# Kernel tuning notes

Measured on AMD Instinct MI355X. Metric: run time of the kernel, lower is better.

The kernel has to match this reference:

```python
import jax, jax.numpy as jnp
import numpy as np

B, T, D, S = 32, 4096, 64, 128


def setup_inputs() -> dict:
    key = jax.random.key(0)
    ks = jax.random.split(key, 6)
    return {
        "observations": jax.random.normal(ks[0], (B, T, D), jnp.float32),
        "trans_logits": jax.random.normal(ks[1], (S, S), jnp.float32),
        "w1": jax.random.normal(ks[2], (4 * S, D), jnp.float32) / np.sqrt(D).astype(np.float32),
        "b1": jnp.zeros((4 * S,), jnp.float32),
        "w2": jax.random.normal(ks[3], (S, 4 * S), jnp.float32) / np.sqrt(4 * S).astype(np.float32),
        "b2": jnp.zeros((S,), jnp.float32),
        "init_logits": jax.random.normal(ks[4], (S,), jnp.float32),
    }


def _hmm_posteriors(observations, trans_logits, w1, b1, w2, b2):
    # observations: (batch, seq, obs_dim) -> (seq, batch, obs_dim)
    obs = jnp.transpose(observations, (1, 0, 2))
    # Emission MLP is time-independent: precompute all emission logits at once.
    hid = jax.nn.relu(jnp.einsum('tbd,hd->tbh', obs, w1) + b1)
    emit = jnp.einsum('tbh,sh->tbs', hid, w2) + b2  # (T, B, S)

    log_trans_f = jax.nn.log_softmax(trans_logits, axis=-1)      # forward cell
    log_trans_b = jax.nn.log_softmax(trans_logits.T, axis=-1)    # backward cell (transposed logits)

    bsz = observations.shape[0]
    n_states = trans_logits.shape[0]
    h0 = jnp.zeros((bsz, n_states), emit.dtype)

    def make_step(log_trans):
        def step(prev, e):
            nxt = jax.scipy.special.logsumexp(prev[:, :, None] + log_trans[None], axis=1) + e
            return nxt, nxt
        return step

    _, log_alphas = jax.lax.scan(make_step(log_trans_f), h0, emit)
    _, betas_rev = jax.lax.scan(make_step(log_trans_b), h0, emit[::-1])
    log_betas = betas_rev[::-1]

    log_Z = jax.scipy.special.logsumexp(log_alphas[-1], axis=-1)  # (B,)
    log_gammas = log_alphas + log_betas - log_Z[None, :, None]
    posteriors = jax.nn.softmax(log_gammas, axis=-1)              # (T, B, S)
    return jnp.transpose(posteriors, (1, 0, 2))                   # (B, T, S)


def reference(observations, trans_logits, w1, b1, w2, b2, init_logits):
    # init_logits is a declared parameter of HMMModel but is unused in forward.
    return _hmm_posteriors(observations, trans_logits, w1, b1, w2, b2)
```

## Files before the change

### kernel.cpp

```cpp
#include <hip/hip_runtime.h>
#include <hip/hip_bf16.h>
#include <stdint.h>

#define BB 32
#define TT 4096
#define DD 64
#define SS 128
#define HH 512

#define SC_W 8
#define SC_L 32

typedef __attribute__((ext_vector_type(4))) float f32x4;
typedef __attribute__((ext_vector_type(8))) short s16x8;
typedef __attribute__((ext_vector_type(4))) short s16x4;

__device__ __forceinline__ ushort f2bfu(float x) {
    uint32_t b = __float_as_uint(x);
    uint32_t r = (b + 0x7FFFu + ((b >> 16) & 1u)) >> 16;
    return (ushort)r;
}
__device__ __forceinline__ float bfu2f(ushort u) {
    return __uint_as_float(((uint32_t)u) << 16);
}

__global__ __launch_bounds__(128) void prep_trans(const float* __restrict__ tr,
                                                  float* __restrict__ PfT,
                                                  float* __restrict__ PbT) {
    int i = blockIdx.x & 127;
    int back = blockIdx.x >> 7;
    int j = threadIdx.x;
    float v = back ? tr[j * SS + i] : tr[i * SS + j];
    __shared__ float sh[4];
    float mx = v;
#pragma unroll
    for (int off = 32; off; off >>= 1) mx = fmaxf(mx, __shfl_xor(mx, off));
    if ((threadIdx.x & 63) == 0) sh[threadIdx.x >> 6] = mx;
    __syncthreads();
    mx = fmaxf(sh[0], sh[1]);
    float e = __expf(v - mx);
    float ssum = e;
#pragma unroll
    for (int off = 32; off; off >>= 1) ssum += __shfl_xor(ssum, off);
    if ((threadIdx.x & 63) == 0) sh[2 + (threadIdx.x >> 6)] = ssum;
    __syncthreads();
    float out = e / (sh[2] + sh[3]);
    if (back) PbT[j * SS + i] = out;
    else      PfT[j * SS + i] = out;
}

__global__ __launch_bounds__(256) void conv_w(const float* __restrict__ w1,
                                              const float* __restrict__ w2,
                                              ushort* __restrict__ w1f,
                                              ushort* __restrict__ w2f) {
    int i = blockIdx.x * 256 + threadIdx.x;
    if (i < 4096) {
        int f1 = i >> 6, l = i & 63;
        int kt = f1 & 1, htile = f1 >> 1;
        int row = htile * 16 + (l & 15);
        int col = kt * 32 + (l >> 4) * 8;
        const float* src = w1 + row * DD + col;
        ushort* dst = w1f + i * 8;
#pragma unroll
        for (int j = 0; j < 8; ++j) dst[j] = f2bfu(src[j]);
    } else if (i < 4096 + 8192) {
        int i2 = i - 4096;
        int f2 = i2 >> 6, l = i2 & 63;
        int kt = f2 & 15, si = (f2 >> 4) & 1, sg = f2 >> 5;
        int row = sg * 32 + si * 16 + (l & 15);
        int col = kt * 32 + (l >> 4) * 8;
        const float* src = w2 + row * HH + col;
        ushort* dst = w2f + i2 * 8;
#pragma unroll
        for (int j = 0; j < 8; ++j) dst[j] = f2bfu(src[j]);
    }
}

#define MLP_ROWS 64
__global__ __launch_bounds__(512, 4) void mlp_kernel(
    const float* __restrict__ obs, const ushort* __restrict__ w1f,
    const ushort* __restrict__ w2f, const float* __restrict__ b1,
    const float* __restrict__ b2, ushort* __restrict__ emitb) {
    __shared__ __align__(16) ushort Alds[MLP_ROWS][72];
    __shared__ __align__(16) ushort Hlds[MLP_ROWS][524];

    int wg = blockIdx.x;
    int bb = wg >> 6;
    int t0 = (wg & 63) * MLP_ROWS;
    int tid = threadIdx.x;
    int lane = tid & 63, wv = tid >> 6;
    int lhi = lane >> 4, llo = lane & 15;

    {
        int r = tid >> 3, c0 = (tid & 7) * 8;
        const float* src = obs + ((size_t)bb * TT + t0 + r) * DD + c0;
        float4 v0 = *(const float4*)(src);
        float4 v1 = *(const float4*)(src + 4);
        s16x8 pk;
        pk[0] = (short)f2bfu(v0.x); pk[1] = (short)f2bfu(v0.y);
        pk[2] = (short)f2bfu(v0.z); pk[3] = (short)f2bfu(v0.w);
        pk[4] = (short)f2bfu(v1.x); pk[5] = (short)f2bfu(v1.y);
        pk[6] = (short)f2bfu(v1.z); pk[7] = (short)f2bfu(v1.w);
        *(s16x8*)(&Alds[r][c0]) = pk;
    }
    __syncthreads();

    int h0 = wv * 64;
    f32x4 acc1[4][4];
#pragma unroll
    for (int mi = 0; mi < 4; ++mi)
#pragma unroll
        for (int nt = 0; nt < 4; ++nt) acc1[mi][nt] = (f32x4){0.f, 0.f, 0.f, 0.f};
#pragma unroll
    for (int kt = 0; kt < 2; ++kt) {
        s16x8 wf1[4];
#pragma unroll
        for (int mi = 0; mi < 4; ++mi) {
            int htile = wv * 4 + mi;
            wf1[mi] = *(const s16x8*)(w1f + ((htile * 2 + kt) * 64 + lane) * 8);
        }
#pragma unroll
        for (int nt = 0; nt < 4; ++nt) {
            s16x8 of = *(const s16x8*)(&Alds[nt * 16 + llo][kt * 32 + lhi * 8]);
#pragma unroll
            for (int mi = 0; mi < 4; ++mi)
                acc1[mi][nt] = __builtin_amdgcn_mfma_f32_16x16x32_bf16(wf1[mi], of, acc1[mi][nt], 0, 0, 0);
        }
    }
#pragma unroll
    for (int mi = 0; mi < 4; ++mi) {
        float4 b1v = *(const float4*)(b1 + h0 + mi * 16 + lhi * 4);
#pragma unroll
        for (int nt = 0; nt < 4; ++nt) {
            s16x4 pk;
            pk[0] = (short)f2bfu(fmaxf(acc1[mi][nt][0] + b1v.x, 0.f));
            pk[1] = (short)f2bfu(fmaxf(acc1[mi][nt][1] + b1v.y, 0.f));
            pk[2] = (short)f2bfu(fmaxf(acc1[mi][nt][2] + b1v.z, 0.f));
            pk[3] = (short)f2bfu(fmaxf(acc1[mi][nt][3] + b1v.w, 0.f));
            *(s16x4*)(&Hlds[nt * 16 + llo][h0 + mi * 16 + lhi * 4]) = pk;
        }
    }

    int sg = wv >> 1, th = wv & 1;
    int sb = sg * 32;
    s16x8 wfr2[4][2];
#pragma unroll
    for (int kp = 0; kp < 4; ++kp)
#pragma unroll
        for (int si = 0; si < 2; ++si)
            wfr2[kp][si] = *(const s16x8*)(w2f + ((sg * 32 + si * 16 + kp) * 64 + lane) * 8);

    __syncthreads();

    f32x4 acc2[2][2];
#pragma unroll
    for (int si = 0; si < 2; ++si)
#pragma unroll
        for (int nt = 0; nt < 2; ++nt) acc2[si][nt] = (f32x4){0.f, 0.f, 0.f, 0.f};
#pragma unroll
    for (int kt = 0; kt < 16; ++kt) {
        s16x8 hf[2];
#pragma unroll
        for (int nt = 0; nt < 2; ++nt)
            hf[nt] = *(const s16x8*)(&Hlds[th * 32 + nt * 16 + llo][kt * 32 + lhi * 8]);
#pragma unroll
        for (int si = 0; si < 2; ++si)
#pragma unroll
            for (int nt = 0; nt < 2; ++nt)
                acc2[si][nt] = __builtin_amdgcn_mfma_f32_16x16x32_bf16(wfr2[kt & 3][si], hf[nt], acc2[si][nt], 0, 0, 0);
        if (kt < 12) {
#pragma unroll
            for (int si = 0; si < 2; ++si)
                wfr2[kt & 3][si] = *(const s16x8*)(w2f + ((sg * 32 + si * 16 + (kt + 4)) * 64 + lane) * 8);
        }
    }
#pragma unroll
    for (int si = 0; si < 2; ++si) {
        int sbase = sb + si * 16 + lhi * 4;
        float4 b2v = *(const float4*)(b2 + sbase);
#pragma unroll
        for (int nt = 0; nt < 2; ++nt) {
            int tl = th * 32 + nt * 16 + llo;
            ushort* dst = emitb + ((size_t)bb * TT + t0 + tl) * SS + sbase;
            s16x4 pk;
            pk[0] = (short)f2bfu(__expf(acc2[si][nt][0] + b2v.x));
            pk[1] = (short)f2bfu(__expf(acc2[si][nt][1] + b2v.y));
            pk[2] = (short)f2bfu(__expf(acc2[si][nt][2] + b2v.z));
            pk[3] = (short)f2bfu(__expf(acc2[si][nt][3] + b2v.w));
            *(s16x4*)dst = pk;
        }
    }
}

__global__ __launch_bounds__(256, 2) void scan_mfma(
    const ushort* __restrict__ Eb, const float* __restrict__ PfT,
    const float* __restrict__ PbT, ushort* __restrict__ galpha,
    ushort* __restrict__ gbeta) {
    int wg = blockIdx.x;
    int b = wg >> 4;
    int dir = (wg >> 3) & 1;
    int wgc = wg & 7;
    int resetRow = (dir == 0) ? (wgc == 0 ? 0 : -1) : (wgc == 7 ? 15 : -1);
    int tid = threadIdx.x;
    int l = tid & 63, w = tid >> 6;
    int l15 = l & 15, g = l >> 4;
    int d = dir ? -1 : 1;

    const float* PT = dir ? PbT : PfT;
    ushort* paB = (dir ? gbeta : galpha) + (size_t)b * TT * SS;
    const ushort* EbB = Eb + (size_t)b * TT * SS;

    int col0 = w * 32 + l15;
    int col1 = col0 + 16;

    s16x8 Bhi[2][4], Blo[2][4];
#pragma unroll
    for (int tile = 0; tile < 2; ++tile) {
        int srow = w * 32 + tile * 16 + l15;
#pragma unroll
        for (int kt = 0; kt < 4; ++kt) {
            const float* src = PT + srow * SS + kt * 32 + g * 8;
            float x[8];
            *(float4*)(x) = *(const float4*)(src);
            *(float4*)(x + 4) = *(const float4*)(src + 4);
            s16x8 hi, lo;
#pragma unroll
            for (int j = 0; j < 8; ++j) {
                uint32_t bx = __float_as_uint(x[j]);
                uint32_t hb = bx & 0xFFFF0000u;
                float rem = x[j] - __uint_as_float(hb);
                hi[j] = (short)(hb >> 16);
                lo[j] = (short)f2bfu(rem);
            }
            Bhi[tile][kt] = hi; Blo[tile][kt] = lo;
        }
    }
#pragma unroll
    for (int tile = 0; tile < 2; ++tile)
#pragma unroll
        for (int kt = 0; kt < 4; ++kt) {
            asm volatile("" : "+v"(Bhi[tile][kt]));
            asm volatile("" : "+v"(Blo[tile][kt]));
        }

    __shared__ __align__(16) ushort Ah[2][16][136];
    __shared__ __align__(16) float mscale[2][16];

    for (int i = tid; i < 16 * 136; i += 256) (&Ah[0][0][0])[i] = (ushort)0x3F80;
    if (tid < 16) mscale[0][tid] = 1.0f;

    int tj[4];
#pragma unroll
    for (int j = 0; j < 4; ++j) {
        int chain = wgc * 16 + 4 * g + j;
        tj[j] = dir ? chain * SC_L + (SC_L - 1) + SC_W : chain * SC_L - SC_W;
    }

    __syncthreads();

    ushort EA[8], EB[8];
#pragma unroll
    for (int j = 0; j < 4; ++j) {
        int tc = tj[j] < 0 ? 0 : (tj[j] > TT - 1 ? TT - 1 : tj[j]);
        uint32_t ro = (uint32_t)tc << 7;
        EA[j] = EbB[ro + col0];
        EA[4 + j] = EbB[ro + col1];
    }

#define SCAN_CORE(par, EC)                                                       \
        s16x8 ahi[4];                                                            \
        _Pragma("unroll") for (int kt = 0; kt < 4; ++kt)                         \
            ahi[kt] = *(const s16x8*)(&Ah[par][l15][kt * 32 + g * 8]);           \
        f32x4 rs = *(const f32x4*)(&mscale[par][4 * g]);                         \
        f32x4 acc0 = {0.f, 0.f, 0.f, 0.f}, acc1 = {0.f, 0.f, 0.f, 0.f};          \
        __builtin_amdgcn_s_setprio(1);                                           \
        _Pragma("unroll") for (int kt = 0; kt < 4; ++kt) {                       \
            acc0 = __builtin_amdgcn_mfma_f32_16x16x32_bf16(ahi[kt], Bhi[0][kt], acc0, 0, 0, 0); \
            acc1 = __builtin_amdgcn_mfma_f32_16x16x32_bf16(ahi[kt], Bhi[1][kt], acc1, 0, 0, 0); \
        }                                                                        \
        _Pragma("unroll") for (int kt = 0; kt < 4; ++kt) {                       \
            acc0 = __builtin_amdgcn_mfma_f32_16x16x32_bf16(ahi[kt], Blo[0][kt], acc0, 0, 0, 0); \
            acc1 = __builtin_amdgcn_mfma_f32_16x16x32_bf16(ahi[kt], Blo[1][kt], acc1, 0, 0, 0); \
        }                                                                        \
        __builtin_amdgcn_s_setprio(0);

#define SCAN_TAIL(par, pv)                                                       \
        _Pragma("unroll") for (int j = 0; j < 4; ++j) {        \
            int rr = 4 * g + j;                                                  \
            Ah[(par) ^ 1][rr][col0] = f2bfu(pv[j]);                              \
            Ah[(par) ^ 1][rr][col1] = f2bfu(pv[4 + j]);                          \
        }                                                                        \
        if (w == 0 && l15 == 0) {                                                \
            f32x4 rn;                                                            \
            _Pragma("unroll") for (int j = 0; j < 4; ++j)                        \
                rn[j] = __builtin_amdgcn_rcpf(pv[j]);                            \
            *(f32x4*)(&mscale[(par) ^ 1][4 * g]) = rn;                           \
        }                                                                        \
        __builtin_amdgcn_sched_barrier(0);                                       \
        asm volatile("s_waitcnt lgkmcnt(0)" ::: "memory");                       \
        __builtin_amdgcn_s_barrier();                                            \
        __builtin_amdgcn_sched_barrier(0);

#define WARM_STEP(VSTEP, par, EC, EN)                                            \
    do {                                                                         \
        _Pragma("unroll") for (int j = 0; j < 4; ++j) {          \
            int tn = tj[j] + d;                                                  \
            int tc = tn < 0 ? 0 : (tn > TT - 1 ? TT - 1 : tn);                   \
            uint32_t ro = (uint32_t)tc << 7;                                     \
            EN[j] = EbB[ro + col0];                                              \
            EN[4 + j] = EbB[ro + col1];                                          \
        }                                                                        \
        SCAN_CORE(par, EC)                                                       \
        float pv[8];                                                             \
        _Pragma("unroll") for (int j = 0; j < 4; ++j) {                          \
            pv[j] = acc0[j] * (bfu2f(EC[j]) * rs[j]);                            \
            pv[4 + j] = acc1[j] * (bfu2f(EC[4 + j]) * rs[j]);                    \
            if ((VSTEP) == SC_W - 1 && resetRow == 4 * g + j) {                  \
                pv[j] = 1.f; pv[4 + j] = 1.f;                                    \
            }                                                                    \
            tj[j] += d;                                                          \
        }                                                                        \
        SCAN_TAIL(par, pv)                                                       \
    } while (0)

#define MAIN_STEP(par, EC, EN)                                                   \
    do {                                                                         \
        _Pragma("unroll") for (int j = 0; j < 4; ++j) {          \
            const char* eb = (const char*)EbB + (ptrdiff_t)vE[j];                \
            EN[j] = *(const ushort*)eb;                                          \
            EN[4 + j] = *(const ushort*)(eb + 32);                               \
            vE[j] += dstepE;                                                     \
        }                                                                        \
        SCAN_CORE(par, EC)                                                       \
        float pv[8];                                                             \
        _Pragma("unroll") for (int j = 0; j < 4; ++j) {                          \
            pv[j] = acc0[j] * (bfu2f(EC[j]) * rs[j]);                            \
            pv[4 + j] = acc1[j] * (bfu2f(EC[4 + j]) * rs[j]);                    \
            char* pb = (char*)paB + vP[j];                                       \
            *(ushort*)pb = f2bfu(pv[j]);                                         \
            *(ushort*)(pb + 32) = f2bfu(pv[4 + j]);                              \
            vP[j] += dstepE;                                                     \
        }                                                                        \
        SCAN_TAIL(par, pv)                                                       \
    } while (0)

    for (int v2 = 0; v2 < SC_W / 2; ++v2) {
        WARM_STEP(2 * v2, 0, EA, EB);
        WARM_STEP(2 * v2 + 1, 1, EB, EA);
    }

    int dstepE = d * 256;
    int vE[4];
    uint32_t vP[4];
#pragma unroll
    for (int j = 0; j < 4; ++j) {
        vE[j] = (tj[j] + d) * 256 + col0 * 2;
        vP[j] = (uint32_t)(tj[j] * 256 + col0 * 2);
    }
    for (int v2 = 0; v2 < SC_L / 2; ++v2) {
        MAIN_STEP(0, EA, EB);
        MAIN_STEP(1, EB, EA);
    }
#undef MAIN_STEP
#undef WARM_STEP
#undef SCAN_TAIL
#undef SCAN_CORE
}

__global__ __launch_bounds__(256) void combine_kernel(
    const ushort* __restrict__ galpha, const ushort* __restrict__ gbeta,
    float* __restrict__ out) {
    int row = blockIdx.x * 4 + (threadIdx.x >> 6);
    int lane = threadIdx.x & 63;
    size_t base = (size_t)row * SS + lane * 2;
    ushort2 a = *(const ushort2*)(galpha + base);
    ushort2 b = *(const ushort2*)(gbeta + base);
    float g0 = bfu2f(a.x) * bfu2f(b.x);
    float g1 = bfu2f(a.y) * bfu2f(b.y);
    float ssum = g0 + g1;
#pragma unroll
    for (int off = 32; off; off >>= 1) ssum += __shfl_xor(ssum, off);
    float inv = 1.f / ssum;
    float2 o; o.x = g0 * inv; o.y = g1 * inv;
    *(float2*)(out + base) = o;
}

extern "C" void kernel_launch(void* const* d_in, const int* in_sizes, int n_in,
                              void* d_out, int out_size, void* d_ws, size_t ws_size,
                              hipStream_t stream) {
    const float* obs = (const float*)d_in[0];
    const float* trans = (const float*)d_in[1];
    const float* w1 = (const float*)d_in[2];
    const float* b1 = (const float*)d_in[3];
    const float* w2 = (const float*)d_in[4];
    const float* b2 = (const float*)d_in[5];

    char* ws = (char*)d_ws;
    float* PfT = (float*)(ws);
    float* PbT = (float*)(ws + 65536);
    ushort* w1f = (ushort*)(ws + 131072);
    ushort* w2f = (ushort*)(ws + 196608);
    ushort* emitb = (ushort*)(ws + 327680);
    ushort* galpha = (ushort*)(ws + 327680 + 33554432);
    ushort* gbeta = (ushort*)(ws + 327680 + 33554432 + 33554432);

    prep_trans<<<256, 128, 0, stream>>>(trans, PfT, PbT);
    conv_w<<<48, 256, 0, stream>>>(w1, w2, w1f, w2f);
    mlp_kernel<<<BB * (TT / MLP_ROWS), 512, 0, stream>>>(obs, w1f, w2f, b1, b2, emitb);
    scan_mfma<<<BB * 2 * 8, 256, 0, stream>>>(emitb, PfT, PbT, galpha, gbeta);
    combine_kernel<<<(BB * TT) / 4, 256, 0, stream>>>(galpha, gbeta, (float*)d_out);
}
```

Baseline: 103.7 us.

## Process two row tiles per MLP block with W1 hoisted and obs prefetch

The emission MLP kernel now handles 128 time steps per workgroup as two 64-row iterations, using half as many blocks. W1 fragments are loaded into registers once and reused across both tiles, and the second tile's observations are prefetched into registers while the first tile is being computed. Launch bounds drop from 4 to 2 blocks per CU, which gives more registers but less occupancy and an extra barrier per iteration. The MLP is only one stage of a pipeline dominated by the sequential scan, so its effect on total time may be limited.

```diff
diff --git a/kernel.cpp b/kernel.cpp
--- a/kernel.cpp
+++ b/kernel.cpp
@@ -77,7 +77,7 @@
 }
 
 #define MLP_ROWS 64
-__global__ __launch_bounds__(512, 4) void mlp_kernel(
+__global__ __launch_bounds__(512, 2) void mlp_kernel(
     const float* __restrict__ obs, const ushort* __restrict__ w1f,
     const ushort* __restrict__ w2f, const float* __restrict__ b1,
     const float* __restrict__ b2, ushort* __restrict__ emitb) {
@@ -85,109 +85,121 @@
     __shared__ __align__(16) ushort Hlds[MLP_ROWS][524];
 
     int wg = blockIdx.x;
-    int bb = wg >> 6;
-    int t0 = (wg & 63) * MLP_ROWS;
+    int bb = wg >> 5;
+    int tp = (wg & 31) * 128;
     int tid = threadIdx.x;
     int lane = tid & 63, wv = tid >> 6;
     int lhi = lane >> 4, llo = lane & 15;
-
-    {
-        int r = tid >> 3, c0 = (tid & 7) * 8;
-        const float* src = obs + ((size_t)bb * TT + t0 + r) * DD + c0;
-        float4 v0 = *(const float4*)(src);
-        float4 v1 = *(const float4*)(src + 4);
-        s16x8 pk;
-        pk[0] = (short)f2bfu(v0.x); pk[1] = (short)f2bfu(v0.y);
-        pk[2] = (short)f2bfu(v0.z); pk[3] = (short)f2bfu(v0.w);
-        pk[4] = (short)f2bfu(v1.x); pk[5] = (short)f2bfu(v1.y);
-        pk[6] = (short)f2bfu(v1.z); pk[7] = (short)f2bfu(v1.w);
-        *(s16x8*)(&Alds[r][c0]) = pk;
-    }
-    __syncthreads();
-
-    int h0 = wv * 64;
-    f32x4 acc1[4][4];
-#pragma unroll
-    for (int mi = 0; mi < 4; ++mi)
-#pragma unroll
-        for (int nt = 0; nt < 4; ++nt) acc1[mi][nt] = (f32x4){0.f, 0.f, 0.f, 0.f};
-#pragma unroll
-    for (int kt = 0; kt < 2; ++kt) {
-        s16x8 wf1[4];
-#pragma unroll
-        for (int mi = 0; mi < 4; ++mi) {
-            int htile = wv * 4 + mi;
-            wf1[mi] = *(const s16x8*)(w1f + ((htile * 2 + kt) * 64 + lane) * 8);
-        }
-#pragma unroll
-        for (int nt = 0; nt < 4; ++nt) {
-            s16x8 of = *(const s16x8*)(&Alds[nt * 16 + llo][kt * 32 + lhi * 8]);
-#pragma unroll
-            for (int mi = 0; mi < 4; ++mi)
-                acc1[mi][nt] = __builtin_amdgcn_mfma_f32_16x16x32_bf16(wf1[mi], of, acc1[mi][nt], 0, 0, 0);
-        }
-    }
-#pragma unroll
-    for (int mi = 0; mi < 4; ++mi) {
-        float4 b1v = *(const float4*)(b1 + h0 + mi * 16 + lhi * 4);
-#pragma unroll
-        for (int nt = 0; nt < 4; ++nt) {
-            s16x4 pk;
-            pk[0] = (short)f2bfu(fmaxf(acc1[mi][nt][0] + b1v.x, 0.f));
-            pk[1] = (short)f2bfu(fmaxf(acc1[mi][nt][1] + b1v.y, 0.f));
-            pk[2] = (short)f2bfu(fmaxf(acc1[mi][nt][2] + b1v.z, 0.f));
-            pk[3] = (short)f2bfu(fmaxf(acc1[mi][nt][3] + b1v.w, 0.f));
-            *(s16x4*)(&Hlds[nt * 16 + llo][h0 + mi * 16 + lhi * 4]) = pk;
-        }
-    }
-
     int sg = wv >> 1, th = wv & 1;
     int sb = sg * 32;
-    s16x8 wfr2[4][2];
-#pragma unroll
-    for (int kp = 0; kp < 4; ++kp)
+    int h0 = wv * 64;
+
+    s16x8 wf1[4][2];
+#pragma unroll
+    for (int mi = 0; mi < 4; ++mi)
+#pragma unroll
+        for (int kt = 0; kt < 2; ++kt)
+            wf1[mi][kt] = *(const s16x8*)(w1f + (((wv * 4 + mi) * 2 + kt) * 64 + lane) * 8);
+
+    int r = tid >> 3, c0 = (tid & 7) * 8;
+    const float* srcA = obs + ((size_t)bb * TT + tp + r) * DD + c0;
+    float4 pv0 = *(const float4*)(srcA);
+    float4 pv1 = *(const float4*)(srcA + 4);
+
+#pragma unroll
+    for (int it = 0; it < 2; ++it) {
+        if (it) __syncthreads();
+        {
+            s16x8 pk;
+            pk[0] = (short)f2bfu(pv0.x); pk[1] = (short)f2bfu(pv0.y);
+            pk[2] = (short)f2bfu(pv0.z); pk[3] = (short)f2bfu(pv0.w);
+            pk[4] = (short)f2bfu(pv1.x); pk[5] = (short)f2bfu(pv1.y);
+            pk[6] = (short)f2bfu(pv1.z); pk[7] = (short)f2bfu(pv1.w);
+            *(s16x8*)(&Alds[r][c0]) = pk;
+        }
+        __syncthreads();
+        if (it == 0) {
+            const float* srcB = srcA + 64 * DD;
+            pv0 = *(const float4*)(srcB);
+            pv1 = *(const float4*)(srcB + 4);
+        }
+        int t0 = tp + it * 64;
+
+        f32x4 acc1[4][4];
+#pragma unroll
+        for (int mi = 0; mi < 4; ++mi)
+#pragma unroll
+            for (int nt = 0; nt < 4; ++nt) acc1[mi][nt] = (f32x4){0.f, 0.f, 0.f, 0.f};
+#pragma unroll
+        for (int kt = 0; kt < 2; ++kt) {
+#pragma unroll
+            for (int nt = 0; nt < 4; ++nt) {
+                s16x8 of = *(const s16x8*)(&Alds[nt * 16 + llo][kt * 32 + lhi * 8]);
+#pragma unroll
+                for (int mi = 0; mi < 4; ++mi)
+                    acc1[mi][nt] = __builtin_amdgcn_mfma_f32_16x16x32_bf16(wf1[mi][kt], of, acc1[mi][nt], 0, 0, 0);
+            }
+        }
+#pragma unroll
+        for (int mi = 0; mi < 4; ++mi) {
+            float4 b1v = *(const float4*)(b1 + h0 + mi * 16 + lhi * 4);
+#pragma unroll
+            for (int nt = 0; nt < 4; ++nt) {
+                s16x4 pk;
+                pk[0] = (short)f2bfu(fmaxf(acc1[mi][nt][0] + b1v.x, 0.f));
+                pk[1] = (short)f2bfu(fmaxf(acc1[mi][nt][1] + b1v.y, 0.f));
+                pk[2] = (short)f2bfu(fmaxf(acc1[mi][nt][2] + b1v.z, 0.f));
+                pk[3] = (short)f2bfu(fmaxf(acc1[mi][nt][3] + b1v.w, 0.f));
+                *(s16x4*)(&Hlds[nt * 16 + llo][h0 + mi * 16 + lhi * 4]) = pk;
+            }
+        }
+
+        s16x8 wfr2[4][2];
+#pragma unroll
+        for (int kp = 0; kp < 4; ++kp)
+#pragma unroll
+            for (int si = 0; si < 2; ++si)
+                wfr2[kp][si] = *(const s16x8*)(w2f + ((sg * 32 + si * 16 + kp) * 64 + lane) * 8);
+
+        __syncthreads();
+
+        f32x4 acc2[2][2];
 #pragma unroll
         for (int si = 0; si < 2; ++si)
-            wfr2[kp][si] = *(const s16x8*)(w2f + ((sg * 32 + si * 16 + kp) * 64 + lane) * 8);
-
-    __syncthreads();
-
-    f32x4 acc2[2][2];
-#pragma unroll
-    for (int si = 0; si < 2; ++si)
-#pragma unroll
-        for (int nt = 0; nt < 2; ++nt) acc2[si][nt] = (f32x4){0.f, 0.f, 0.f, 0.f};
-#pragma unroll
-    for (int kt = 0; kt < 16; ++kt) {
-        s16x8 hf[2];
-#pragma unroll
-        for (int nt = 0; nt < 2; ++nt)
-            hf[nt] = *(const s16x8*)(&Hlds[th * 32 + nt * 16 + llo][kt * 32 + lhi * 8]);
-#pragma unroll
-        for (int si = 0; si < 2; ++si)
+#pragma unroll
+            for (int nt = 0; nt < 2; ++nt) acc2[si][nt] = (f32x4){0.f, 0.f, 0.f, 0.f};
+#pragma unroll
+        for (int kt = 0; kt < 16; ++kt) {
+            s16x8 hf[2];
 #pragma unroll
             for (int nt = 0; nt < 2; ++nt)
-                acc2[si][nt] = __builtin_amdgcn_mfma_f32_16x16x32_bf16(wfr2[kt & 3][si], hf[nt], acc2[si][nt], 0, 0, 0);
-        if (kt < 12) {
+                hf[nt] = *(const s16x8*)(&Hlds[th * 32 + nt * 16 + llo][kt * 32 + lhi * 8]);
 #pragma unroll
             for (int si = 0; si < 2; ++si)
-                wfr2[kt & 3][si] = *(const s16x8*)(w2f + ((sg * 32 + si * 16 + (kt + 4)) * 64 + lane) * 8);
-        }
-    }
-#pragma unroll
-    for (int si = 0; si < 2; ++si) {
-        int sbase = sb + si * 16 + lhi * 4;
-        float4 b2v = *(const float4*)(b2 + sbase);
-#pragma unroll
-        for (int nt = 0; nt < 2; ++nt) {
-            int tl = th * 32 + nt * 16 + llo;
-            ushort* dst = emitb + ((size_t)bb * TT + t0 + tl) * SS + sbase;
-            s16x4 pk;
-            pk[0] = (short)f2bfu(__expf(acc2[si][nt][0] + b2v.x));
-            pk[1] = (short)f2bfu(__expf(acc2[si][nt][1] + b2v.y));
-            pk[2] = (short)f2bfu(__expf(acc2[si][nt][2] + b2v.z));
-            pk[3] = (short)f2bfu(__expf(acc2[si][nt][3] + b2v.w));
-            *(s16x4*)dst = pk;
+#pragma unroll
+                for (int nt = 0; nt < 2; ++nt)
+                    acc2[si][nt] = __builtin_amdgcn_mfma_f32_16x16x32_bf16(wfr2[kt & 3][si], hf[nt], acc2[si][nt], 0, 0, 0);
+            if (kt < 12) {
+#pragma unroll
+                for (int si = 0; si < 2; ++si)
+                    wfr2[kt & 3][si] = *(const s16x8*)(w2f + ((sg * 32 + si * 16 + (kt + 4)) * 64 + lane) * 8);
+            }
+        }
+#pragma unroll
+        for (int si = 0; si < 2; ++si) {
+            int sbase = sb + si * 16 + lhi * 4;
+            float4 b2v = *(const float4*)(b2 + sbase);
+#pragma unroll
+            for (int nt = 0; nt < 2; ++nt) {
+                int tl = th * 32 + nt * 16 + llo;
+                ushort* dst = emitb + ((size_t)bb * TT + t0 + tl) * SS + sbase;
+                s16x4 pk;
+                pk[0] = (short)f2bfu(__expf(acc2[si][nt][0] + b2v.x));
+                pk[1] = (short)f2bfu(__expf(acc2[si][nt][1] + b2v.y));
+                pk[2] = (short)f2bfu(__expf(acc2[si][nt][2] + b2v.z));
+                pk[3] = (short)f2bfu(__expf(acc2[si][nt][3] + b2v.w));
+                *(s16x4*)dst = pk;
+            }
         }
     }
 }
@@ -406,7 +418,7 @@
 
     prep_trans<<<256, 128, 0, stream>>>(trans, PfT, PbT);
     conv_w<<<48, 256, 0, stream>>>(w1, w2, w1f, w2f);
-    mlp_kernel<<<BB * (TT / MLP_ROWS), 512, 0, stream>>>(obs, w1f, w2f, b1, b2, emitb);
+    mlp_kernel<<<BB * (TT / 128), 512, 0, stream>>>(obs, w1f, w2f, b1, b2, emitb);
     scan_mfma<<<BB * 2 * 8, 256, 0, stream>>>(emitb, PfT, PbT, galpha, gbeta);
     combine_kernel<<<(BB * TT) / 4, 256, 0, stream>>>(galpha, gbeta, (float*)d_out);
 }
```

Measured after the change: 108.4 us. 1.05x slower.
